# Performance work log

Hardware: AMD Instinct MI355X
Metric: run time of the kernel (lower is better)

The kernel has to match this reference:

```python
import jax, jax.numpy as jnp
import numpy as np

B, T, N = 32, 1024, 256
D = 1024          # latent_dim
TD = 768          # text_latent_dim
H = 16            # num_head
C = D // H        # head dim
TE = 2048         # time_embed_dim
EPS = 1e-5


def layer_norm(x, g, b):
    mu = jnp.mean(x, axis=-1, keepdims=True)
    var = jnp.var(x, axis=-1, keepdims=True)
    return (x - mu) * jax.lax.rsqrt(var + EPS) * g + b


def setup_inputs() -> dict:
    key = jax.random.key(0)
    ks = jax.random.split(key, 16)
    s_d = 1.0 / np.sqrt(D)
    s_td = 1.0 / np.sqrt(TD)
    s_te = 1.0 / np.sqrt(TE)
    return {
        "x": jax.random.normal(ks[0], (B, T, D), jnp.float32),
        "xf": jax.random.normal(ks[1], (B, N, TD), jnp.float32),
        "emb": jax.random.normal(ks[2], (B, TE), jnp.float32),
        "norm_g": jnp.ones((D,), jnp.float32),
        "norm_b": jnp.zeros((D,), jnp.float32),
        "tnorm_g": jnp.ones((TD,), jnp.float32),
        "tnorm_b": jnp.zeros((TD,), jnp.float32),
        "Wq": jax.random.normal(ks[3], (D, D), jnp.float32) * s_d,
        "bq": jnp.zeros((D,), jnp.float32),
        "Wk": jax.random.normal(ks[4], (TD, D), jnp.float32) * s_td,
        "bk": jnp.zeros((D,), jnp.float32),
        "Wv": jax.random.normal(ks[5], (TD, D), jnp.float32) * s_td,
        "bv": jnp.zeros((D,), jnp.float32),
        "emb_W": jax.random.normal(ks[6], (TE, 2 * D), jnp.float32) * s_te,
        "emb_b": jnp.zeros((2 * D,), jnp.float32),
        "fnorm_g": jnp.ones((D,), jnp.float32),
        "fnorm_b": jnp.zeros((D,), jnp.float32),
        "out_W": jax.random.normal(ks[7], (D, D), jnp.float32) * s_d,
        "out_b": jnp.zeros((D,), jnp.float32),
    }


def reference(x, xf, emb, norm_g, norm_b, tnorm_g, tnorm_b, Wq, bq, Wk, bk, Wv, bv,
              emb_W, emb_b, fnorm_g, fnorm_b, out_W, out_b):
    # projections from normalized inputs
    xn = layer_norm(x, norm_g, norm_b)            # [B,T,D]
    xfn = layer_norm(xf, tnorm_g, tnorm_b)        # [B,N,TD]
    q = (xn @ Wq + bq).reshape(B, T, H, C)        # [B,T,H,C]
    k = (xfn @ Wk + bk).reshape(B, N, H, C)       # [B,N,H,C]
    v = (xfn @ Wv + bv).reshape(B, N, H, C)       # [B,N,H,C]
    # dual softmax: query over channel dim, key over sequence dim
    q = jax.nn.softmax(q, axis=-1)
    k = jax.nn.softmax(k, axis=1)
    # linear attention: attn = k^T v over sequence, then q @ attn
    attn = jnp.einsum('bnhc,bnhd->bhcd', k, v)    # [B,H,C,C]
    y = jnp.einsum('bthc,bhcd->bthd', q, attn).reshape(B, T, D)
    # FiLM / StylizationBlock (dropout = identity at eval)
    e = jax.nn.silu(emb) @ emb_W + emb_b          # [B,2D]
    scale, shift = jnp.split(e[:, None, :], 2, axis=2)
    h = layer_norm(y, fnorm_g, fnorm_b) * (1.0 + scale) + shift
    h = jax.nn.silu(h) @ out_W + out_b
    return x + h
```

## Files before the change

kernel.cpp:

```cpp
#include <hip/hip_runtime.h>
#include <hip/hip_bf16.h>
#include <stdint.h>

#define B_  32
#define T_  1024
#define N_  256
#define D_  1024
#define TD_ 768
#define H_  16
#define C_  64
#define TE_ 2048

typedef __bf16 bf16x8 __attribute__((ext_vector_type(8)));
typedef __bf16 bf16x4 __attribute__((ext_vector_type(4)));
typedef float  f32x4  __attribute__((ext_vector_type(4)));

__device__ __forceinline__ void gll16(const void* g, void* l) {
  __builtin_amdgcn_global_load_lds(
      (const __attribute__((address_space(1))) unsigned int*)g,
      (__attribute__((address_space(3))) unsigned int*)l, 16, 0, 0);
}

__global__ void fill_val(float* o, float v, int n) {
  int i = blockIdx.x * 256 + threadIdx.x;
  if (i < n) o[i] = v;
}

__global__ void concat2(const float* __restrict__ a, const float* __restrict__ b,
                        float* __restrict__ o) {
  int i = blockIdx.x * 256 + threadIdx.x;
  if (i < 1024) o[i] = a[i];
  else if (i < 2048) o[i] = b[i - 1024];
}

__global__ void transpose_cast(const float* __restrict__ in,
                               __bf16* __restrict__ out, int R, int C) {
  __shared__ float t[32][33];
  int c0 = blockIdx.x * 32, r0 = blockIdx.y * 32;
  int x = threadIdx.x, y4 = threadIdx.y;
#pragma unroll
  for (int i = 0; i < 4; i++) {
    int rr = y4 * 4 + i;
    t[rr][x] = in[(size_t)(r0 + rr) * C + c0 + x];
  }
  __syncthreads();
#pragma unroll
  for (int i = 0; i < 4; i++) {
    int rr = y4 * 4 + i;
    out[(size_t)(c0 + rr) * R + r0 + x] = (__bf16)t[x][rr];
  }
}

__global__ __launch_bounds__(256)
void ln1024(const float* __restrict__ x, const float* __restrict__ g,
            const float* __restrict__ bb, __bf16* __restrict__ out) {
  size_t row = blockIdx.x;
  int c4 = threadIdx.x * 4;
  f32x4 v = *(const f32x4*)(x + row * D_ + c4);
  float s = v[0] + v[1] + v[2] + v[3];
  float s2 = v[0]*v[0] + v[1]*v[1] + v[2]*v[2] + v[3]*v[3];
#pragma unroll
  for (int off = 32; off; off >>= 1) {
    s += __shfl_down(s, off);
    s2 += __shfl_down(s2, off);
  }
  __shared__ float red[8];
  int wave = threadIdx.x >> 6, lane = threadIdx.x & 63;
  if (lane == 0) { red[wave] = s; red[4 + wave] = s2; }
  __syncthreads();
  if (threadIdx.x == 0) {
    float a = 0.f, c = 0.f;
    for (int w = 0; w < 4; w++) { a += red[w]; c += red[4 + w]; }
    red[0] = a; red[4] = c;
  }
  __syncthreads();
  float mu = red[0] / D_;
  float var = red[4] / D_ - mu * mu;
  float rstd = rsqrtf(var + 1e-5f);
  f32x4 gg = *(const f32x4*)(g + c4);
  f32x4 bbv = *(const f32x4*)(bb + c4);
  bf16x4 o;
#pragma unroll
  for (int t = 0; t < 4; t++) o[t] = (__bf16)((v[t] - mu) * rstd * gg[t] + bbv[t]);
  *(bf16x4*)(out + row * D_ + c4) = o;
}

__global__ __launch_bounds__(256)
void ln_rows(const float* __restrict__ x, const float* __restrict__ g,
             const float* __restrict__ bb, __bf16* __restrict__ out, int D) {
  size_t row = blockIdx.x;
  const float* xr = x + row * (size_t)D;
  int tid = threadIdx.x;
  int cnt = D >> 8;
  float v[4];
  float s = 0.f, s2 = 0.f;
  for (int i = 0; i < cnt; i++) {
    float f = xr[tid + i * 256];
    v[i] = f; s += f; s2 += f * f;
  }
#pragma unroll
  for (int off = 32; off; off >>= 1) {
    s += __shfl_down(s, off);
    s2 += __shfl_down(s2, off);
  }
  __shared__ float red[8];
  int wave = tid >> 6, lane = tid & 63;
  if (lane == 0) { red[wave] = s; red[4 + wave] = s2; }
  __syncthreads();
  if (tid == 0) {
    float a = 0.f, c = 0.f;
    for (int w = 0; w < 4; w++) { a += red[w]; c += red[4 + w]; }
    red[0] = a; red[4] = c;
  }
  __syncthreads();
  float mu = red[0] / D;
  float var = red[4] / D - mu * mu;
  float rstd = rsqrtf(var + 1e-5f);
  for (int i = 0; i < cnt; i++) {
    int c = tid + i * 256;
    out[row * (size_t)D + c] = (__bf16)((v[i] - mu) * rstd * g[c] + bb[c]);
  }
}

#define SYNCV_(n)                                                  \
  do {                                                             \
    __builtin_amdgcn_sched_barrier(0);                             \
    asm volatile("s_waitcnt vmcnt(" #n ")\n\ts_barrier" ::: "memory"); \
  } while (0)
#define SYNCV(n) SYNCV_(n)

template <int EPI, typename CT>
__global__ __launch_bounds__(512, 2)
void gemm256(const __bf16* __restrict__ A, const __bf16* __restrict__ BT,
             const float* __restrict__ bias, const float* __restrict__ res,
             CT* __restrict__ C, int M, int N, int K, int NT) {
  __shared__ char smem[131072];
  const int tid = threadIdx.x;
  const int ln = tid & 63, wv = tid >> 6;

  const int nwg = gridDim.x;
  const int swz = (blockIdx.x & 7) * (nwg >> 3) + (blockIdx.x >> 3);
  const int m0 = (swz / NT) * 256, n0 = (swz % NT) * 256;

  const int wm = (wv >> 2) * 128, wn = (wv & 3) * 64;
  const int lr = ln & 15;
  const int xorv = (lr & 7) << 4;
  const int k16 = (ln >> 4) * 16;
  const int koff0 = k16 ^ xorv;
  const int koff1 = (64 + k16) ^ xorv;

  const int brow = tid >> 3;
  const int bseg = (tid & 7) ^ (brow & 7);
  const __bf16* Bg = BT + (size_t)(n0 + brow) * K + bseg * 8;
  const int ahalf = tid >> 8, au = tid & 255;
  const int arow = au >> 3;
  const int aseg = (au & 7) ^ (arow & 7);
  const __bf16* Ag = A + (size_t)(m0 + ahalf * 128 + arow) * K + aseg * 8;

  char* sBstage = smem + wv * 1024;
  char* sAstage = smem + 32768 + ahalf * 16384 + (wv & 3) * 1024;

  const int nt = K >> 6;
  f32x4 acc[8][4] = {};
  bf16x8 bfr[4][2], af[2][2];

#define STAGE_B(bf, s, k0) \
  gll16(Bg + (size_t)(s) * 64 * K + (k0), sBstage + (bf) * 65536 + (s) * 8192)
#define STAGE_A(bf, p, k0) \
  gll16(Ag + (size_t)(p) * 32 * K + (k0), sAstage + (bf) * 65536 + (p) * 4096)
#define LDA(pp, ar, kf) \
  (*(const bf16x8*)(sArd + ((wm + (pp) * 32 + (ar) * 16 + lr) * 128) + (kf)))

#define DO_MFMA(pp)                                                          \
  do {                                                                       \
    __builtin_amdgcn_s_setprio(1);                                           \
    _Pragma("unroll") for (int ar = 0; ar < 2; ++ar) {                       \
      _Pragma("unroll") for (int j = 0; j < 4; ++j) {                        \
        acc[(pp) * 2 + ar][j] = __builtin_amdgcn_mfma_f32_16x16x32_bf16(     \
            af[ar][0], bfr[j][0], acc[(pp) * 2 + ar][j], 0, 0, 0);           \
        acc[(pp) * 2 + ar][j] = __builtin_amdgcn_mfma_f32_16x16x32_bf16(     \
            af[ar][1], bfr[j][1], acc[(pp) * 2 + ar][j], 0, 0, 0);           \
      }                                                                      \
    }                                                                        \
    __builtin_amdgcn_s_setprio(0);                                           \
  } while (0)

#define TILE(buf, kst, PF, w0, w1, w2, w3)                                   \
  do {                                                                       \
    const char* sBrd = smem + (buf) * 65536;                                 \
    const char* sArd = sBrd + 32768;                                         \
    SYNCV(w0);                                                               \
    if (PF) { STAGE_B((buf) ^ 1, 0, kst); STAGE_B((buf) ^ 1, 1, kst); }      \
    _Pragma("unroll") for (int j = 0; j < 4; ++j) {                          \
      bfr[j][0] = *(const bf16x8*)(sBrd + (wn + j * 16 + lr) * 128 + koff0); \
      bfr[j][1] = *(const bf16x8*)(sBrd + (wn + j * 16 + lr) * 128 + koff1); \
    }                                                                        \
    af[0][0] = LDA(0, 0, koff0); af[0][1] = LDA(0, 0, koff1);                \
    af[1][0] = LDA(0, 1, koff0); af[1][1] = LDA(0, 1, koff1);                \
    DO_MFMA(0);                                                              \
    SYNCV(w1);                                                               \
    if (PF) { STAGE_B((buf) ^ 1, 2, kst); STAGE_B((buf) ^ 1, 3, kst); }      \
    af[0][0] = LDA(1, 0, koff0); af[0][1] = LDA(1, 0, koff1);                \
    af[1][0] = LDA(1, 1, koff0); af[1][1] = LDA(1, 1, koff1);                \
    DO_MFMA(1);                                                              \
    SYNCV(w2);                                                               \
    if (PF) { STAGE_A((buf) ^ 1, 0, kst); STAGE_A((buf) ^ 1, 1, kst); }      \
    af[0][0] = LDA(2, 0, koff0); af[0][1] = LDA(2, 0, koff1);                \
    af[1][0] = LDA(2, 1, koff0); af[1][1] = LDA(2, 1, koff1);                \
    DO_MFMA(2);                                                              \
    SYNCV(w3);                                                               \
    if (PF) { STAGE_A((buf) ^ 1, 2, kst); STAGE_A((buf) ^ 1, 3, kst); }      \
    af[0][0] = LDA(3, 0, koff0); af[0][1] = LDA(3, 0, koff1);                \
    af[1][0] = LDA(3, 1, koff0); af[1][1] = LDA(3, 1, koff1);                \
    DO_MFMA(3);                                                              \
  } while (0)

  STAGE_B(0, 0, 0); STAGE_B(0, 1, 0); STAGE_B(0, 2, 0); STAGE_B(0, 3, 0);
  STAGE_A(0, 0, 0); STAGE_A(0, 1, 0); STAGE_A(0, 2, 0); STAGE_A(0, 3, 0);

  int kst = 64;
  const int npair = (nt >> 1) - 1;
  for (int tt = 0; tt < npair; ++tt) {
    TILE(0, kst, 1, 3, 4, 5, 6); kst += 64;
    TILE(1, kst, 1, 3, 4, 5, 6); kst += 64;
  }
  TILE(0, kst, 1, 3, 4, 5, 6);
  TILE(1, 0, 0, 3, 2, 1, 0);

#undef TILE
#undef DO_MFMA
#undef LDA
#undef STAGE_A
#undef STAGE_B

  __syncthreads();
  float* scratch = (float*)smem + wv * 1088;
  const int qd = ln >> 4;
#pragma unroll
  for (int i = 0; i < 8; ++i) {
#pragma unroll
    for (int j = 0; j < 4; ++j)
#pragma unroll
      for (int r = 0; r < 4; ++r)
        scratch[(qd * 4 + r) * 68 + j * 16 + lr] = acc[i][j][r];
    asm volatile("s_waitcnt lgkmcnt(0)" ::: "memory");
#pragma unroll
    for (int s = 0; s < 4; ++s) {
      int rr = qd + 4 * s;
      f32x4 vv = *(f32x4*)&scratch[rr * 68 + lr * 4];
      int row = m0 + wm + i * 16 + rr;
      int col = n0 + wn + lr * 4;
      size_t idx = (size_t)row * N + col;
      vv += *(const f32x4*)&bias[col];
      if (EPI == 1) vv += *(const f32x4*)&res[idx];
      if constexpr (sizeof(CT) == 4) {
        *(f32x4*)&C[idx] = vv;
      } else {
        bf16x4 o;
#pragma unroll
        for (int t2 = 0; t2 < 4; ++t2) o[t2] = (__bf16)vv[t2];
        *(bf16x4*)&C[idx] = o;
      }
    }
    asm volatile("s_waitcnt lgkmcnt(0)" ::: "memory");
  }
}

__global__ __launch_bounds__(256)
void kv_attn(const __bf16* __restrict__ kv, float* __restrict__ attn) {
  int h = blockIdx.x & 15, b = blockIdx.x >> 4;
  __shared__ __bf16 sK[256 * 72];
  __shared__ float sV[32 * 64];
  __shared__ float sInv[64];
  int tid = threadIdx.x;
  const __bf16* kb = kv + (size_t)b * N_ * 2048 + h * C_;
  const __bf16* vb = kb + 1024;

  {
    const __bf16* src = kb + (size_t)tid * 2048;
#pragma unroll
    for (int j = 0; j < 8; j++)
      *(bf16x8*)&sK[tid * 72 + j * 8] = *(const bf16x8*)(src + j * 8);
  }
  __syncthreads();

  {
    int c = tid >> 2, qq = tid & 3;
    float m = -1e30f;
    for (int t = 0; t < 64; t++)
      m = fmaxf(m, (float)sK[(qq * 64 + t) * 72 + c]);
    m = fmaxf(m, __shfl_xor(m, 1));
    m = fmaxf(m, __shfl_xor(m, 2));
    float s = 0.f;
    for (int t = 0; t < 64; t++) {
      int idx = (qq * 64 + t) * 72 + c;
      float e = __expf((float)sK[idx] - m);
      sK[idx] = (__bf16)e;
      s += e;
    }
    s += __shfl_xor(s, 1);
    s += __shfl_xor(s, 2);
    if (qq == 0) sInv[c] = 1.f / s;
  }
  __syncthreads();

  int c0 = (tid & 15) * 4, d0 = (tid >> 4) * 4;
  float acc[4][4] = {};
  for (int n0 = 0; n0 < N_; n0 += 32) {
    __syncthreads();
    {
      int r = tid >> 3, s8 = (tid & 7) * 8;
      bf16x8 vv8 = *(const bf16x8*)(vb + (size_t)(n0 + r) * 2048 + s8);
#pragma unroll
      for (int j = 0; j < 8; j++) sV[r * 64 + s8 + j] = (float)vv8[j];
    }
    __syncthreads();
    for (int n = 0; n < 32; n++) {
      bf16x4 kk = *(const bf16x4*)&sK[(n0 + n) * 72 + c0];
      f32x4 vd = *(const f32x4*)&sV[n * 64 + d0];
#pragma unroll
      for (int i = 0; i < 4; i++) {
        float kf = (float)kk[i];
#pragma unroll
        for (int j = 0; j < 4; j++) acc[i][j] += kf * vd[j];
      }
    }
  }
  float* ab = attn + (size_t)(b * H_ + h) * 4096;
#pragma unroll
  for (int i = 0; i < 4; i++) {
    float inv = sInv[c0 + i];
    f32x4 o;
#pragma unroll
    for (int j = 0; j < 4; j++) o[j] = acc[i][j] * inv;
    *(f32x4*)&ab[(c0 + i) * 64 + d0] = o;
  }
}

__global__ __launch_bounds__(256)
void qattn_y(const __bf16* __restrict__ q, const float* __restrict__ attn,
             __bf16* __restrict__ y) {
  int tt = blockIdx.x * 64;
  int h = blockIdx.y, b = blockIdx.z;
  __shared__ float sQ[64 * 65];
  __shared__ float sA[64 * 64];
  int tid = threadIdx.x;
  const __bf16* qb = q + ((size_t)b * T_ + tt) * D_ + h * C_;
#pragma unroll
  for (int it = 0; it < 2; it++) {
    int r = (tid >> 3) + it * 32;
    int cc = (tid & 7) * 8;
    bf16x8 vv = *(const bf16x8*)(qb + (size_t)r * D_ + cc);
#pragma unroll
    for (int j = 0; j < 8; j++) sQ[(cc + j) * 65 + r] = (float)vv[j];
  }
  const float* ab = attn + (size_t)(b * H_ + h) * 4096;
  for (int i = tid; i < 1024; i += 256) ((f32x4*)sA)[i] = ((const f32x4*)ab)[i];
  __syncthreads();
  {
    int r = tid >> 2, sub = tid & 3;
    float m = -1e30f;
#pragma unroll
    for (int j = 0; j < 16; j++)
      m = fmaxf(m, sQ[(sub * 16 + j) * 65 + r]);
    m = fmaxf(m, __shfl_xor(m, 1));
    m = fmaxf(m, __shfl_xor(m, 2));
    float s = 0.f;
#pragma unroll
    for (int j = 0; j < 16; j++) {
      int idx = (sub * 16 + j) * 65 + r;
      float e = __expf(sQ[idx] - m);
      sQ[idx] = e;
      s += e;
    }
    s += __shfl_xor(s, 1);
    s += __shfl_xor(s, 2);
    float inv = 1.f / s;
#pragma unroll
    for (int j = 0; j < 16; j++) sQ[(sub * 16 + j) * 65 + r] *= inv;
  }
  __syncthreads();
  int r0 = (tid >> 4) * 4, d0 = (tid & 15) * 4;
  float acc[4][4] = {};
  for (int c = 0; c < 64; c++) {
    f32x4 qv = *(const f32x4*)&sQ[c * 65 + r0];
    f32x4 av = *(const f32x4*)&sA[c * 64 + d0];
#pragma unroll
    for (int i = 0; i < 4; i++)
#pragma unroll
      for (int j = 0; j < 4; j++) acc[i][j] += qv[i] * av[j];
  }
  __bf16* yb = y + ((size_t)b * T_ + tt) * D_ + h * C_;
#pragma unroll
  for (int i = 0; i < 4; i++) {
    bf16x4 o;
#pragma unroll
    for (int j = 0; j < 4; j++) o[j] = (__bf16)acc[i][j];
    *(bf16x4*)(yb + (size_t)(r0 + i) * D_ + d0) = o;
  }
}

__global__ __launch_bounds__(256)
void emb_gemm(const float* __restrict__ emb, const float* __restrict__ W,
              const float* __restrict__ eb, float* __restrict__ ss) {
  int b = blockIdx.x >> 3;
  int n = (blockIdx.x & 7) * 256 + threadIdx.x;
  __shared__ float se[TE_];
  for (int i = threadIdx.x; i < TE_; i += 256) {
    float xv = emb[(size_t)b * TE_ + i];
    se[i] = xv / (1.f + __expf(-xv));
  }
  __syncthreads();
  float acc = 0.f;
  for (int kk = 0; kk < TE_; kk++) acc += se[kk] * W[(size_t)kk * 2048 + n];
  ss[(size_t)b * 2048 + n] = acc + eb[n];
}

__global__ __launch_bounds__(256)
void film_rows(const __bf16* __restrict__ y, const float* __restrict__ ss,
               const float* __restrict__ g, const float* __restrict__ bb,
               __bf16* __restrict__ out) {
  size_t row = blockIdx.x;
  int b = (int)(row >> 10);
  int c4 = threadIdx.x * 4;
  bf16x4 yv = *(const bf16x4*)(y + row * D_ + c4);
  float v[4];
  float s = 0.f, s2 = 0.f;
#pragma unroll
  for (int t = 0; t < 4; t++) {
    v[t] = (float)yv[t];
    s += v[t]; s2 += v[t] * v[t];
  }
#pragma unroll
  for (int off = 32; off; off >>= 1) {
    s += __shfl_down(s, off);
    s2 += __shfl_down(s2, off);
  }
  __shared__ float red[8];
  int wave = threadIdx.x >> 6, lane = threadIdx.x & 63;
  if (lane == 0) { red[wave] = s; red[4 + wave] = s2; }
  __syncthreads();
  if (threadIdx.x == 0) {
    float a = 0.f, c = 0.f;
    for (int w = 0; w < 4; w++) { a += red[w]; c += red[4 + w]; }
    red[0] = a; red[4] = c;
  }
  __syncthreads();
  float mu = red[0] / D_;
  float var = red[4] / D_ - mu * mu;
  float rstd = rsqrtf(var + 1e-5f);
  f32x4 gg = *(const f32x4*)(g + c4);
  f32x4 bbv = *(const f32x4*)(bb + c4);
  f32x4 sc = *(const f32x4*)(ss + (size_t)b * 2048 + c4);
  f32x4 sh = *(const f32x4*)(ss + (size_t)b * 2048 + 1024 + c4);
  bf16x4 o;
#pragma unroll
  for (int t = 0; t < 4; t++) {
    float ln = (v[t] - mu) * rstd * gg[t] + bbv[t];
    float hh = ln * (1.f + sc[t]) + sh[t];
    o[t] = (__bf16)(hh / (1.f + __expf(-hh)));
  }
  *(bf16x4*)(out + row * D_ + c4) = o;
}

extern "C" void kernel_launch(void* const* d_in, const int* in_sizes, int n_in,
                              void* d_out, int out_size, void* d_ws,
                              size_t ws_size, hipStream_t stream) {
  (void)in_sizes; (void)n_in;
  const float* x       = (const float*)d_in[0];
  const float* xf      = (const float*)d_in[1];
  const float* emb     = (const float*)d_in[2];
  const float* norm_g  = (const float*)d_in[3];
  const float* norm_b  = (const float*)d_in[4];
  const float* tnorm_g = (const float*)d_in[5];
  const float* tnorm_b = (const float*)d_in[6];
  const float* Wq      = (const float*)d_in[7];
  const float* bq      = (const float*)d_in[8];
  const float* Wk      = (const float*)d_in[9];
  const float* bk      = (const float*)d_in[10];
  const float* Wv      = (const float*)d_in[11];
  const float* bv      = (const float*)d_in[12];
  const float* emb_W   = (const float*)d_in[13];
  const float* emb_b   = (const float*)d_in[14];
  const float* fnorm_g = (const float*)d_in[15];
  const float* fnorm_b = (const float*)d_in[16];
  const float* out_W   = (const float*)d_in[17];
  const float* out_b   = (const float*)d_in[18];
  float* out = (float*)d_out;

  const size_t SZ_WQT  = (size_t)D_ * D_ * 2;
  const size_t SZ_WKVT = (size_t)2048 * TD_ * 2;
  const size_t SZ_XN   = (size_t)B_ * T_ * D_ * 2;
  const size_t SZ_XFN  = (size_t)B_ * N_ * TD_ * 2;
  const size_t SZ_KV   = (size_t)B_ * N_ * 2048 * 2;
  const size_t SZ_BKV  = 2048 * 4;
  const size_t NEED = SZ_WQT * 2 + SZ_WKVT + SZ_XN + SZ_XFN + SZ_KV + SZ_BKV;

  if (ws_size < NEED) {
    fill_val<<<(out_size + 255) / 256, 256, 0, stream>>>(
        out, (float)(ws_size >> 20), out_size);
    return;
  }

  char* w = (char*)d_ws;
  __bf16* WqT  = (__bf16*)w; w += SZ_WQT;
  __bf16* WkvT = (__bf16*)w; w += SZ_WKVT;
  __bf16* WoT  = (__bf16*)w; w += SZ_WQT;
  __bf16* xn   = (__bf16*)w; w += SZ_XN;
  char*   xfnR = w;          w += SZ_XFN;
  __bf16* kvbuf= (__bf16*)w; w += SZ_KV;
  float*  bkv  = (float*)w;  w += SZ_BKV;
  __bf16* xfn  = (__bf16*)xfnR;
  float*  attn = (float*)xfnR;
  float*  ss   = (float*)(xfnR + (size_t)B_ * H_ * C_ * C_ * 4);
  __bf16* hpre = xn;
  __bf16* qbuf = (__bf16*)out;
  __bf16* ybuf = qbuf;

  transpose_cast<<<dim3(D_ / 32, D_ / 32), dim3(32, 8), 0, stream>>>(Wq, WqT, D_, D_);
  transpose_cast<<<dim3(D_ / 32, TD_ / 32), dim3(32, 8), 0, stream>>>(Wk, WkvT, TD_, D_);
  transpose_cast<<<dim3(D_ / 32, TD_ / 32), dim3(32, 8), 0, stream>>>(
      Wv, WkvT + (size_t)1024 * TD_, TD_, D_);
  transpose_cast<<<dim3(D_ / 32, D_ / 32), dim3(32, 8), 0, stream>>>(out_W, WoT, D_, D_);
  concat2<<<8, 256, 0, stream>>>(bk, bv, bkv);

  ln1024<<<B_ * T_, 256, 0, stream>>>(x, norm_g, norm_b, xn);
  ln_rows<<<B_ * N_, 256, 0, stream>>>(xf, tnorm_g, tnorm_b, xfn, TD_);

  gemm256<0, __bf16><<<dim3((B_ * T_ / 256) * (D_ / 256)), 512, 0, stream>>>(
      xn, WqT, bq, nullptr, qbuf, B_ * T_, D_, D_, D_ / 256);
  gemm256<0, __bf16><<<dim3((B_ * N_ / 256) * (2048 / 256)), 512, 0, stream>>>(
      xfn, WkvT, bkv, nullptr, kvbuf, B_ * N_, 2048, TD_, 2048 / 256);

  kv_attn<<<B_ * H_, 256, 0, stream>>>(kvbuf, attn);

  qattn_y<<<dim3(T_ / 64, H_, B_), 256, 0, stream>>>(qbuf, attn, ybuf);

  emb_gemm<<<B_ * 8, 256, 0, stream>>>(emb, emb_W, emb_b, ss);
  film_rows<<<B_ * T_, 256, 0, stream>>>(ybuf, ss, fnorm_g, fnorm_b, hpre);

  gemm256<1, float><<<dim3((B_ * T_ / 256) * (D_ / 256)), 512, 0, stream>>>(
      hpre, WoT, out_b, x, out, B_ * T_, D_, D_, D_ / 256);
}
```

Measured before the change: 728.3 us.

## Merge preprocessing, dual GEMMs and attention/embedding kernels into fewer launches

Collapses the weight transposes, bias concat, both layer norms and the scale/shift bias init into one block-indexed preprocess kernel. The Q and KV projection GEMMs now share a single launch, and the emb GEMM is split over K with atomicAdd and runs inside the k^T v attention kernel. The attention inner tile grows from 32 to 64 rows. The goal is to cut launch gaps and tail underutilization from many small kernels. The cost is atomics, extra branching in each kernel, and a larger shared-memory footprint in attn_emb that can lower its occupancy.

```diff
diff --git a/kernel.cpp b/kernel.cpp
--- a/kernel.cpp
+++ b/kernel.cpp
@@ -26,18 +26,11 @@
   if (i < n) o[i] = v;
 }
 
-__global__ void concat2(const float* __restrict__ a, const float* __restrict__ b,
-                        float* __restrict__ o) {
-  int i = blockIdx.x * 256 + threadIdx.x;
-  if (i < 1024) o[i] = a[i];
-  else if (i < 2048) o[i] = b[i - 1024];
-}
-
-__global__ void transpose_cast(const float* __restrict__ in,
-                               __bf16* __restrict__ out, int R, int C) {
-  __shared__ float t[32][33];
-  int c0 = blockIdx.x * 32, r0 = blockIdx.y * 32;
-  int x = threadIdx.x, y4 = threadIdx.y;
+__device__ __forceinline__ void tc_block(const float* __restrict__ in,
+                                         __bf16* __restrict__ out, int R, int C,
+                                         int bx, int by, int x, int y4,
+                                         float (*t)[33]) {
+  int c0 = bx * 32, r0 = by * 32;
 #pragma unroll
   for (int i = 0; i < 4; i++) {
     int rr = y4 * 4 + i;
@@ -52,73 +45,110 @@
 }
 
 __global__ __launch_bounds__(256)
-void ln1024(const float* __restrict__ x, const float* __restrict__ g,
-            const float* __restrict__ bb, __bf16* __restrict__ out) {
-  size_t row = blockIdx.x;
-  int c4 = threadIdx.x * 4;
-  f32x4 v = *(const f32x4*)(x + row * D_ + c4);
-  float s = v[0] + v[1] + v[2] + v[3];
-  float s2 = v[0]*v[0] + v[1]*v[1] + v[2]*v[2] + v[3]*v[3];
-#pragma unroll
-  for (int off = 32; off; off >>= 1) {
-    s += __shfl_down(s, off);
-    s2 += __shfl_down(s2, off);
-  }
+void preprocess(const float* __restrict__ Wq, const float* __restrict__ Wk,
+                const float* __restrict__ Wv, const float* __restrict__ Wo,
+                const float* __restrict__ bk, const float* __restrict__ bv,
+                const float* __restrict__ x, const float* __restrict__ ng,
+                const float* __restrict__ nb, const float* __restrict__ xf,
+                const float* __restrict__ tg, const float* __restrict__ tb,
+                const float* __restrict__ eb,
+                __bf16* __restrict__ WqT, __bf16* __restrict__ WkvT,
+                __bf16* __restrict__ WoT, float* __restrict__ bkv,
+                __bf16* __restrict__ xn, __bf16* __restrict__ xfn,
+                float* __restrict__ ss) {
+  __shared__ float t[32][33];
   __shared__ float red[8];
-  int wave = threadIdx.x >> 6, lane = threadIdx.x & 63;
-  if (lane == 0) { red[wave] = s; red[4 + wave] = s2; }
-  __syncthreads();
-  if (threadIdx.x == 0) {
-    float a = 0.f, c = 0.f;
-    for (int w = 0; w < 4; w++) { a += red[w]; c += red[4 + w]; }
-    red[0] = a; red[4] = c;
-  }
-  __syncthreads();
-  float mu = red[0] / D_;
-  float var = red[4] / D_ - mu * mu;
-  float rstd = rsqrtf(var + 1e-5f);
-  f32x4 gg = *(const f32x4*)(g + c4);
-  f32x4 bbv = *(const f32x4*)(bb + c4);
-  bf16x4 o;
-#pragma unroll
-  for (int t = 0; t < 4; t++) o[t] = (__bf16)((v[t] - mu) * rstd * gg[t] + bbv[t]);
-  *(bf16x4*)(out + row * D_ + c4) = o;
-}
-
-__global__ __launch_bounds__(256)
-void ln_rows(const float* __restrict__ x, const float* __restrict__ g,
-             const float* __restrict__ bb, __bf16* __restrict__ out, int D) {
-  size_t row = blockIdx.x;
-  const float* xr = x + row * (size_t)D;
-  int tid = threadIdx.x;
-  int cnt = D >> 8;
-  float v[4];
-  float s = 0.f, s2 = 0.f;
-  for (int i = 0; i < cnt; i++) {
-    float f = xr[tid + i * 256];
-    v[i] = f; s += f; s2 += f * f;
-  }
-#pragma unroll
-  for (int off = 32; off; off >>= 1) {
-    s += __shfl_down(s, off);
-    s2 += __shfl_down(s2, off);
-  }
-  __shared__ float red[8];
-  int wave = tid >> 6, lane = tid & 63;
-  if (lane == 0) { red[wave] = s; red[4 + wave] = s2; }
-  __syncthreads();
-  if (tid == 0) {
-    float a = 0.f, c = 0.f;
-    for (int w = 0; w < 4; w++) { a += red[w]; c += red[4 + w]; }
-    red[0] = a; red[4] = c;
-  }
-  __syncthreads();
-  float mu = red[0] / D;
-  float var = red[4] / D - mu * mu;
-  float rstd = rsqrtf(var + 1e-5f);
-  for (int i = 0; i < cnt; i++) {
-    int c = tid + i * 256;
-    out[row * (size_t)D + c] = (__bf16)((v[i] - mu) * rstd * g[c] + bb[c]);
+  int bid = blockIdx.x, tid = threadIdx.x;
+  int xq = tid & 31, y4 = tid >> 5;
+
+  if (bid < 1024) { tc_block(Wq, WqT, D_, D_, bid & 31, bid >> 5, xq, y4, t); return; }
+  bid -= 1024;
+  if (bid < 768) { tc_block(Wk, WkvT, TD_, D_, bid & 31, bid >> 5, xq, y4, t); return; }
+  bid -= 768;
+  if (bid < 768) {
+    tc_block(Wv, WkvT + (size_t)1024 * TD_, TD_, D_, bid & 31, bid >> 5, xq, y4, t);
+    return;
+  }
+  bid -= 768;
+  if (bid < 1024) { tc_block(Wo, WoT, D_, D_, bid & 31, bid >> 5, xq, y4, t); return; }
+  bid -= 1024;
+  if (bid < 8) {
+    int i = bid * 256 + tid;
+    if (i < 1024) bkv[i] = bk[i];
+    else bkv[i] = bv[i - 1024];
+    return;
+  }
+  bid -= 8;
+  if (bid < 32768) {
+    size_t row = bid;
+    int c4 = tid * 4;
+    f32x4 v = *(const f32x4*)(x + row * D_ + c4);
+    float s = v[0] + v[1] + v[2] + v[3];
+    float s2 = v[0]*v[0] + v[1]*v[1] + v[2]*v[2] + v[3]*v[3];
+#pragma unroll
+    for (int off = 32; off; off >>= 1) {
+      s += __shfl_down(s, off);
+      s2 += __shfl_down(s2, off);
+    }
+    int wave = tid >> 6, lane = tid & 63;
+    if (lane == 0) { red[wave] = s; red[4 + wave] = s2; }
+    __syncthreads();
+    if (tid == 0) {
+      float a = 0.f, c = 0.f;
+      for (int w = 0; w < 4; w++) { a += red[w]; c += red[4 + w]; }
+      red[0] = a; red[4] = c;
+    }
+    __syncthreads();
+    float mu = red[0] / D_;
+    float var = red[4] / D_ - mu * mu;
+    float rstd = rsqrtf(var + 1e-5f);
+    f32x4 gg = *(const f32x4*)(ng + c4);
+    f32x4 bbv = *(const f32x4*)(nb + c4);
+    bf16x4 o;
+#pragma unroll
+    for (int q = 0; q < 4; q++) o[q] = (__bf16)((v[q] - mu) * rstd * gg[q] + bbv[q]);
+    *(bf16x4*)(xn + row * D_ + c4) = o;
+    return;
+  }
+  bid -= 32768;
+  if (bid < 8192) {
+    size_t row = bid;
+    const float* xr = xf + row * (size_t)TD_;
+    float v[3];
+    float s = 0.f, s2 = 0.f;
+#pragma unroll
+    for (int i = 0; i < 3; i++) {
+      float f = xr[tid + i * 256];
+      v[i] = f; s += f; s2 += f * f;
+    }
+#pragma unroll
+    for (int off = 32; off; off >>= 1) {
+      s += __shfl_down(s, off);
+      s2 += __shfl_down(s2, off);
+    }
+    int wave = tid >> 6, lane = tid & 63;
+    if (lane == 0) { red[wave] = s; red[4 + wave] = s2; }
+    __syncthreads();
+    if (tid == 0) {
+      float a = 0.f, c = 0.f;
+      for (int w = 0; w < 4; w++) { a += red[w]; c += red[4 + w]; }
+      red[0] = a; red[4] = c;
+    }
+    __syncthreads();
+    float mu = red[0] / TD_;
+    float var = red[4] / TD_ - mu * mu;
+    float rstd = rsqrtf(var + 1e-5f);
+#pragma unroll
+    for (int i = 0; i < 3; i++) {
+      int c = tid + i * 256;
+      xfn[row * (size_t)TD_ + c] = (__bf16)((v[i] - mu) * rstd * tg[c] + tb[c]);
+    }
+    return;
+  }
+  bid -= 8192;
+  {
+    int i = bid * 256 + tid;
+    ss[i] = eb[i & 2047];
   }
 }
 
@@ -130,16 +160,15 @@
 #define SYNCV(n) SYNCV_(n)
 
 template <int EPI, typename CT>
-__global__ __launch_bounds__(512, 2)
-void gemm256(const __bf16* __restrict__ A, const __bf16* __restrict__ BT,
-             const float* __restrict__ bias, const float* __restrict__ res,
-             CT* __restrict__ C, int M, int N, int K, int NT) {
-  __shared__ char smem[131072];
+__device__ __forceinline__ void gemm_body(char* smem,
+    const __bf16* __restrict__ A, const __bf16* __restrict__ BT,
+    const float* __restrict__ bias, const float* __restrict__ res,
+    CT* __restrict__ C, int K, int NT, int bid, int nwg) {
   const int tid = threadIdx.x;
   const int ln = tid & 63, wv = tid >> 6;
-
-  const int nwg = gridDim.x;
-  const int swz = (blockIdx.x & 7) * (nwg >> 3) + (blockIdx.x >> 3);
+  const int N = NT << 8;
+
+  const int swz = (bid & 7) * (nwg >> 3) + (bid >> 3);
   const int m0 = (swz / NT) * 256, n0 = (swz % NT) * 256;
 
   const int wm = (wv >> 2) * 128, wn = (wv & 3) * 64;
@@ -266,13 +295,61 @@
   }
 }
 
+__global__ __launch_bounds__(512, 2)
+void gemm_dual(const __bf16* __restrict__ A0, const __bf16* __restrict__ B0,
+               const float* __restrict__ bias0, __bf16* __restrict__ C0,
+               int K0, int NT0, int n0,
+               const __bf16* __restrict__ A1, const __bf16* __restrict__ B1,
+               const float* __restrict__ bias1, __bf16* __restrict__ C1,
+               int K1, int NT1) {
+  __shared__ char smem[131072];
+  int bid = blockIdx.x;
+  if (bid < n0)
+    gemm_body<0, __bf16>(smem, A0, B0, bias0, nullptr, C0, K0, NT0, bid, n0);
+  else
+    gemm_body<0, __bf16>(smem, A1, B1, bias1, nullptr, C1, K1, NT1, bid - n0,
+                         (int)gridDim.x - n0);
+}
+
+__global__ __launch_bounds__(512, 2)
+void gemm_ep(const __bf16* __restrict__ A, const __bf16* __restrict__ BT,
+             const float* __restrict__ bias, const float* __restrict__ res,
+             float* __restrict__ C, int K, int NT) {
+  __shared__ char smem[131072];
+  gemm_body<1, float>(smem, A, BT, bias, res, C, K, NT, blockIdx.x,
+                      (int)gridDim.x);
+}
+
 __global__ __launch_bounds__(256)
-void kv_attn(const __bf16* __restrict__ kv, float* __restrict__ attn) {
+void attn_emb(const __bf16* __restrict__ kv, float* __restrict__ attn,
+              const float* __restrict__ emb, const float* __restrict__ W,
+              float* __restrict__ ss) {
+  __shared__ __bf16 sK[256 * 72];
+  __shared__ float sV[64 * 64];
+  __shared__ float sInv[64];
+  __shared__ float se[512];
+  int tid = threadIdx.x;
+
+  if (blockIdx.x >= 512) {
+    int bid = blockIdx.x - 512;
+    int b  = bid >> 5;
+    int nc = (bid >> 2) & 7;
+    int kq = bid & 3;
+    int k0 = kq * 512;
+    for (int i = tid; i < 512; i += 256) {
+      float xv = emb[(size_t)b * TE_ + k0 + i];
+      se[i] = xv / (1.f + __expf(-xv));
+    }
+    __syncthreads();
+    int n = nc * 256 + tid;
+    float acc = 0.f;
+    for (int kk = 0; kk < 512; kk++)
+      acc += se[kk] * W[(size_t)(k0 + kk) * 2048 + n];
+    atomicAdd(&ss[(size_t)b * 2048 + n], acc);
+    return;
+  }
+
   int h = blockIdx.x & 15, b = blockIdx.x >> 4;
-  __shared__ __bf16 sK[256 * 72];
-  __shared__ float sV[32 * 64];
-  __shared__ float sInv[64];
-  int tid = threadIdx.x;
   const __bf16* kb = kv + (size_t)b * N_ * 2048 + h * C_;
   const __bf16* vb = kb + 1024;
 
@@ -306,16 +383,21 @@
 
   int c0 = (tid & 15) * 4, d0 = (tid >> 4) * 4;
   float acc[4][4] = {};
-  for (int n0 = 0; n0 < N_; n0 += 32) {
+  for (int n0 = 0; n0 < N_; n0 += 64) {
     __syncthreads();
     {
-      int r = tid >> 3, s8 = (tid & 7) * 8;
-      bf16x8 vv8 = *(const bf16x8*)(vb + (size_t)(n0 + r) * 2048 + s8);
-#pragma unroll
-      for (int j = 0; j < 8; j++) sV[r * 64 + s8 + j] = (float)vv8[j];
+      int r = tid >> 2, s8 = (tid & 3) * 16;
+      const __bf16* vr = vb + (size_t)(n0 + r) * 2048 + s8;
+      bf16x8 a0 = *(const bf16x8*)vr;
+      bf16x8 a1 = *(const bf16x8*)(vr + 8);
+#pragma unroll
+      for (int j = 0; j < 8; j++) {
+        sV[r * 64 + s8 + j] = (float)a0[j];
+        sV[r * 64 + s8 + 8 + j] = (float)a1[j];
+      }
     }
     __syncthreads();
-    for (int n = 0; n < 32; n++) {
+    for (int n = 0; n < 64; n++) {
       bf16x4 kk = *(const bf16x4*)&sK[(n0 + n) * 72 + c0];
       f32x4 vd = *(const f32x4*)&sV[n * 64 + d0];
 #pragma unroll
@@ -398,22 +480,6 @@
     for (int j = 0; j < 4; j++) o[j] = (__bf16)acc[i][j];
     *(bf16x4*)(yb + (size_t)(r0 + i) * D_ + d0) = o;
   }
-}
-
-__global__ __launch_bounds__(256)
-void emb_gemm(const float* __restrict__ emb, const float* __restrict__ W,
-              const float* __restrict__ eb, float* __restrict__ ss) {
-  int b = blockIdx.x >> 3;
-  int n = (blockIdx.x & 7) * 256 + threadIdx.x;
-  __shared__ float se[TE_];
-  for (int i = threadIdx.x; i < TE_; i += 256) {
-    float xv = emb[(size_t)b * TE_ + i];
-    se[i] = xv / (1.f + __expf(-xv));
-  }
-  __syncthreads();
-  float acc = 0.f;
-  for (int kk = 0; kk < TE_; kk++) acc += se[kk] * W[(size_t)kk * 2048 + n];
-  ss[(size_t)b * 2048 + n] = acc + eb[n];
 }
 
 __global__ __launch_bounds__(256)
@@ -494,7 +560,9 @@
   const size_t SZ_XFN  = (size_t)B_ * N_ * TD_ * 2;
   const size_t SZ_KV   = (size_t)B_ * N_ * 2048 * 2;
   const size_t SZ_BKV  = 2048 * 4;
-  const size_t NEED = SZ_WQT * 2 + SZ_WKVT + SZ_XN + SZ_XFN + SZ_KV + SZ_BKV;
+  const size_t SZ_SS   = (size_t)B_ * 2048 * 4;
+  const size_t NEED =
+      SZ_WQT * 2 + SZ_WKVT + SZ_XN + SZ_XFN + SZ_KV + SZ_BKV + SZ_SS;
 
   if (ws_size < NEED) {
     fill_val<<<(out_size + 255) / 256, 256, 0, stream>>>(
@@ -510,35 +578,26 @@
   char*   xfnR = w;          w += SZ_XFN;
   __bf16* kvbuf= (__bf16*)w; w += SZ_KV;
   float*  bkv  = (float*)w;  w += SZ_BKV;
+  float*  ss   = (float*)w;  w += SZ_SS;
   __bf16* xfn  = (__bf16*)xfnR;
   float*  attn = (float*)xfnR;
-  float*  ss   = (float*)(xfnR + (size_t)B_ * H_ * C_ * C_ * 4);
   __bf16* hpre = xn;
   __bf16* qbuf = (__bf16*)out;
   __bf16* ybuf = qbuf;
 
-  transpose_cast<<<dim3(D_ / 32, D_ / 32), dim3(32, 8), 0, stream>>>(Wq, WqT, D_, D_);
-  transpose_cast<<<dim3(D_ / 32, TD_ / 32), dim3(32, 8), 0, stream>>>(Wk, WkvT, TD_, D_);
-  transpose_cast<<<dim3(D_ / 32, TD_ / 32), dim3(32, 8), 0, stream>>>(
-      Wv, WkvT + (size_t)1024 * TD_, TD_, D_);
-  transpose_cast<<<dim3(D_ / 32, D_ / 32), dim3(32, 8), 0, stream>>>(out_W, WoT, D_, D_);
-  concat2<<<8, 256, 0, stream>>>(bk, bv, bkv);
-
-  ln1024<<<B_ * T_, 256, 0, stream>>>(x, norm_g, norm_b, xn);
-  ln_rows<<<B_ * N_, 256, 0, stream>>>(xf, tnorm_g, tnorm_b, xfn, TD_);
-
-  gemm256<0, __bf16><<<dim3((B_ * T_ / 256) * (D_ / 256)), 512, 0, stream>>>(
-      xn, WqT, bq, nullptr, qbuf, B_ * T_, D_, D_, D_ / 256);
-  gemm256<0, __bf16><<<dim3((B_ * N_ / 256) * (2048 / 256)), 512, 0, stream>>>(
-      xfn, WkvT, bkv, nullptr, kvbuf, B_ * N_, 2048, TD_, 2048 / 256);
-
-  kv_attn<<<B_ * H_, 256, 0, stream>>>(kvbuf, attn);
+  preprocess<<<44808, 256, 0, stream>>>(Wq, Wk, Wv, out_W, bk, bv,
+                                        x, norm_g, norm_b, xf, tnorm_g,
+                                        tnorm_b, emb_b,
+                                        WqT, WkvT, WoT, bkv, xn, xfn, ss);
+
+  gemm_dual<<<768, 512, 0, stream>>>(xn, WqT, bq, qbuf, D_, D_ / 256, 512,
+                                     xfn, WkvT, bkv, kvbuf, TD_, 2048 / 256);
+
+  attn_emb<<<1536, 256, 0, stream>>>(kvbuf, attn, emb, emb_W, ss);
 
   qattn_y<<<dim3(T_ / 64, H_, B_), 256, 0, stream>>>(qbuf, attn, ybuf);
 
-  emb_gemm<<<B_ * 8, 256, 0, stream>>>(emb, emb_W, emb_b, ss);
   film_rows<<<B_ * T_, 256, 0, stream>>>(ybuf, ss, fnorm_g, fnorm_b, hpre);
 
-  gemm256<1, float><<<dim3((B_ * T_ / 256) * (D_ / 256)), 512, 0, stream>>>(
-      hpre, WoT, out_b, x, out, B_ * T_, D_, D_, D_ / 256);
-}
+  gemm_ep<<<512, 512, 0, stream>>>(hpre, WoT, out_b, x, out, D_, D_ / 256);
+}
```

Measured after the change: 637.4 us. -12.5%, faster.
